# Kernel optimization log

Hardware: AMD Instinct MI355X
Metric: run time of the kernel (lower is better)

## Reference

```python
import jax, jax.numpy as jnp
import numpy as np

N, E, D, G = 50000, 600000, 128, 512  # nodes, edges, embed_dim, graphs-per-batch
LN_EPS = 1e-5


def setup_inputs() -> dict:
    key = jax.random.key(0)
    ks = jax.random.split(key, 8)
    node_hidden = jax.random.normal(ks[0], (N, D), dtype=jnp.float32)
    edge_hidden = jax.random.normal(ks[1], (E, D), dtype=jnp.float32)
    # GINEConv MLP params: Linear(D, 2D) -> ReLU -> Linear(2D, D)
    W1 = jax.random.normal(ks[2], (D, 2 * D), dtype=jnp.float32) * (1.0 / np.sqrt(D))
    b1 = jnp.zeros((2 * D,), dtype=jnp.float32)
    W2 = jax.random.normal(ks[3], (2 * D, D), dtype=jnp.float32) * (1.0 / np.sqrt(2 * D))
    b2 = jnp.zeros((D,), dtype=jnp.float32)
    ln_gamma = jnp.ones((D,), dtype=jnp.float32)
    ln_beta = jnp.zeros((D,), dtype=jnp.float32)
    edge_index = jax.random.randint(ks[4], (2, E), 0, N, dtype=jnp.int32)
    node_id = jnp.sort(jax.random.randint(ks[5], (N,), 0, G, dtype=jnp.int32))
    edge_id = jnp.sort(jax.random.randint(ks[6], (E,), 0, G, dtype=jnp.int32))
    return {
        "node_hidden": node_hidden, "edge_hidden": edge_hidden,
        "W1": W1, "b1": b1, "W2": W2, "b2": b2,
        "ln_gamma": ln_gamma, "ln_beta": ln_beta,
        "edge_index": edge_index, "node_id": node_id, "edge_id": edge_id,
    }


def reference(node_hidden, edge_hidden, W1, b1, W2, b2, ln_gamma, ln_beta,
              edge_index, node_id, edge_id):
    n = node_hidden.shape[0]
    src, dst = edge_index[0], edge_index[1]
    # --- GINEConv: msg = relu(x_src + e), scatter-add at dst, (1+eps)*x + agg, MLP ---
    msg = jax.nn.relu(node_hidden[src] + edge_hidden)          # [E, D]
    agg = jax.ops.segment_sum(msg, dst, num_segments=n)        # [N, D]
    h = node_hidden + agg                                      # eps = 0 (PyG default)
    h = jax.nn.relu(jnp.dot(h, W1) + b1)
    h = jnp.dot(h, W2) + b2                                    # [N, D]
    # --- LayerNorm over feature dim ---
    mu = jnp.mean(h, axis=-1, keepdims=True)
    var = jnp.mean(jnp.square(h - mu), axis=-1, keepdims=True)
    h = (h - mu) * jax.lax.rsqrt(var + LN_EPS) * ln_gamma + ln_beta
    # --- GraphNorm: divide each node's features by sqrt(#nodes in its graph) ---
    counts = jax.ops.segment_sum(jnp.ones((n,), dtype=h.dtype), node_id,
                                 num_segments=G)               # [G]
    scale = jax.lax.rsqrt(jnp.maximum(counts, 1.0))            # [G]
    h = h * scale[node_id][:, None]
    # --- last_act=True -> ReLU; dropout is identity in eval; residual add ---
    h = jax.nn.relu(h)
    return h + node_hidden
```

## Files before the change

kernel.cpp:

```cpp
#include <hip/hip_runtime.h>
#include <hip/hip_bf16.h>

#define N_NODES 50000
#define N_EDGES 600000
#define DIM     128
#define HID     256
#define NGRAPH  512
#define LN_EPS  1e-5f
#define CAP     48

typedef __attribute__((ext_vector_type(8))) short bf16x8;
typedef __attribute__((ext_vector_type(4))) float f32x4;

__device__ __forceinline__ unsigned short f2bf(float x) {
  unsigned int u = __builtin_bit_cast(unsigned int, x);
  unsigned int r = (u + 0x7FFFu + ((u >> 16) & 1u)) >> 16;
  return (unsigned short)r;
}

__global__ void k_init_prep(const float* __restrict__ W1, const float* __restrict__ W2,
                            unsigned char* __restrict__ blob,
                            int* __restrict__ deg, int* __restrict__ counts) {
  int id = blockIdx.x * 256 + threadIdx.x;
  if (id < N_NODES) deg[id] = 0;
  if (id < NGRAPH) counts[id] = 0;
  union { unsigned short s[8]; uint4 v; } u;
  if (id < 4096) {
    int c  = id >> 4;
    int k0 = (id & 15) * 8;
#pragma unroll
    for (int j = 0; j < 8; ++j) u.s[j] = f2bf(W1[(size_t)(k0 + j) * HID + c]);
    unsigned char* dst = blob + c * 256 + ((k0 * 2) ^ ((c & 7) << 4));
    *(uint4*)dst = u.v;
  } else if (id < 8192) {
    int id2 = id - 4096;
    int c  = id2 >> 5;
    int k0 = (id2 & 31) * 8;
#pragma unroll
    for (int j = 0; j < 8; ++j) u.s[j] = f2bf(W2[(size_t)(k0 + j) * DIM + c]);
    unsigned char* dst = blob + 65536 + c * 512 + ((k0 * 2) ^ ((c & 7) << 4));
    *(uint4*)dst = u.v;
  }
}

__global__ void k_scatter(const int* __restrict__ ei, const int* __restrict__ node_id,
                          int* __restrict__ deg, int2* __restrict__ slots2,
                          int* __restrict__ counts) {
  int t = blockIdx.x * 256 + threadIdx.x;
  if (t < N_NODES) atomicAdd(&counts[node_id[t]], 1);
  if (t < N_EDGES) {
    int src = ei[t];
    int dst = ei[N_EDGES + t];
    int pos = atomicAdd(&deg[dst], 1);
    if (pos < CAP) slots2[(size_t)dst * CAP + pos] = make_int2(t, src);
  }
}

__global__ __launch_bounds__(512) void k_gather(
    const f32x4* __restrict__ nh4, const f32x4* __restrict__ eh4,
    const int* __restrict__ deg, const int2* __restrict__ slots2,
    f32x4* __restrict__ out4) {
  const int lane = threadIdx.x & 63;
  const int wave = threadIdx.x >> 6;
  const int l31  = lane & 31;
  const int half = lane >> 5;
  const int nbase = (blockIdx.x * 8 + wave) * 4;

  int dcur = 0;
  int2 scur = make_int2(0, 0);
  if (nbase < N_NODES) {
    dcur = deg[nbase];
    if (lane < CAP) scur = slots2[(size_t)nbase * CAP + lane];
  }
#pragma unroll
  for (int p = 0; p < 4; ++p) {
    int node = nbase + p;
    if (node >= N_NODES) break;
    int d = min(dcur, CAP);
    int2 s = scur;
    if (p < 3) {
      int nn = nbase + p + 1;
      if (nn < N_NODES) {
        dcur = deg[nn];
        if (lane < CAP) scur = slots2[(size_t)nn * CAP + lane];
      } else {
        dcur = 0;
      }
    }
    f32x4 acc = (f32x4){0.f, 0.f, 0.f, 0.f};
    if (half == 0) acc = nh4[(size_t)node * 32 + l31];
    int nloop = (d + 1) >> 1;
#pragma unroll 4
    for (int i = 0; i < nloop; ++i) {
      int idx = 2 * i + half;
      int ee = __shfl(s.x, idx);
      int ss = __shfl(s.y, idx);
      if (idx < d) {
        f32x4 x = nh4[(size_t)ss * 32 + l31];
        f32x4 y = __builtin_nontemporal_load(&eh4[(size_t)ee * 32 + l31]);
        acc.x += fmaxf(x.x + y.x, 0.f);
        acc.y += fmaxf(x.y + y.y, 0.f);
        acc.z += fmaxf(x.z + y.z, 0.f);
        acc.w += fmaxf(x.w + y.w, 0.f);
      }
    }
    acc.x += __shfl_xor(acc.x, 32);
    acc.y += __shfl_xor(acc.y, 32);
    acc.z += __shfl_xor(acc.z, 32);
    acc.w += __shfl_xor(acc.w, 32);
    if (half == 0) out4[(size_t)node * 32 + l31] = acc;
  }
}

__global__ __launch_bounds__(512, 2) void k_mlp(
    const float* acc, const float* __restrict__ nh,
    const unsigned char* __restrict__ blob,
    const float* __restrict__ b1v, const float* __restrict__ b2v,
    const float* __restrict__ gam, const float* __restrict__ bet,
    const int* __restrict__ node_id, const int* __restrict__ counts,
    float* outp) {
  __shared__ unsigned char lds[131072];
  const int tid  = threadIdx.x;
  const int lane = tid & 63;
  const int wave = tid >> 6;
  const int l15  = lane & 15;
  const int lhi  = lane >> 4;
  const int swz  = (lane & 7) << 4;

  {
    const uint4* s = (const uint4*)blob;
    uint4* d = (uint4*)lds;
#pragma unroll
    for (int i = 0; i < 16; ++i) d[tid + i * 512] = s[tid + i * 512];
  }
  __syncthreads();

  const int row0 = blockIdx.x * 128 + wave * 16;
  const int arow = row0 + l15;
  const bool aok = arow < N_NODES;
  const float* ap = acc + (size_t)arow * DIM + lhi * 8;

  f32x4 c1[16];
#pragma unroll
  for (int i = 0; i < 16; ++i) c1[i] = (f32x4){0.f, 0.f, 0.f, 0.f};

#pragma unroll
  for (int ks = 0; ks < 4; ++ks) {
    bf16x8 af;
    if (aok) {
      float4 x0 = *(const float4*)(ap + ks * 32);
      float4 x1 = *(const float4*)(ap + ks * 32 + 4);
      af[0] = (short)f2bf(x0.x);
      af[1] = (short)f2bf(x0.y);
      af[2] = (short)f2bf(x0.z);
      af[3] = (short)f2bf(x0.w);
      af[4] = (short)f2bf(x1.x);
      af[5] = (short)f2bf(x1.y);
      af[6] = (short)f2bf(x1.z);
      af[7] = (short)f2bf(x1.w);
    } else {
#pragma unroll
      for (int j = 0; j < 8; ++j) af[j] = 0;
    }
#pragma unroll
    for (int ct = 0; ct < 16; ++ct) {
      int c = ct * 16 + l15;
      const bf16x8* bp = (const bf16x8*)(lds + c * 256 + ((ks * 64 + lhi * 16) ^ swz));
      c1[ct] = __builtin_amdgcn_mfma_f32_16x16x32_bf16(af, *bp, c1[ct], 0, 0, 0);
    }
  }
  __syncthreads();

  unsigned char* hb = lds + wave * 8192;
#pragma unroll
  for (int ct = 0; ct < 16; ++ct) {
    int c = ct * 16 + l15;
    float bb = b1v[c];
#pragma unroll
    for (int i = 0; i < 4; ++i) {
      int r = lhi * 4 + i;
      float v = fmaxf(c1[ct][i] + bb, 0.f);
      *(unsigned short*)(hb + r * 512 + ((2 * c) ^ ((r & 7) << 4))) = f2bf(v);
    }
  }
  __syncthreads();

  f32x4 c2[8];
#pragma unroll
  for (int i = 0; i < 8; ++i) c2[i] = (f32x4){0.f, 0.f, 0.f, 0.f};

#pragma unroll
  for (int ks = 0; ks < 8; ++ks) {
    bf16x8 af = *(const bf16x8*)(hb + l15 * 512 + ((ks * 64 + lhi * 16) ^ swz));
#pragma unroll
    for (int ct = 0; ct < 8; ++ct) {
      int c = ct * 16 + l15;
      const bf16x8* bp = (const bf16x8*)(lds + 65536 + c * 512 + ((ks * 64 + lhi * 16) ^ swz));
      c2[ct] = __builtin_amdgcn_mfma_f32_16x16x32_bf16(af, *bp, c2[ct], 0, 0, 0);
    }
  }

  float vbuf[8][4];
  float s[4] = {0.f, 0.f, 0.f, 0.f}, sq[4] = {0.f, 0.f, 0.f, 0.f};
#pragma unroll
  for (int ct = 0; ct < 8; ++ct) {
    float bb = b2v[ct * 16 + l15];
#pragma unroll
    for (int i = 0; i < 4; ++i) {
      float x = c2[ct][i] + bb;
      vbuf[ct][i] = x;
      s[i] += x;
      sq[i] += x * x;
    }
  }
#pragma unroll
  for (int m = 1; m <= 8; m <<= 1) {
#pragma unroll
    for (int i = 0; i < 4; ++i) {
      s[i] += __shfl_xor(s[i], m, 64);
      sq[i] += __shfl_xor(sq[i], m, 64);
    }
  }
  float mu[4], rstd[4], gs[4];
  int rr[4];
  bool rok[4];
#pragma unroll
  for (int i = 0; i < 4; ++i) {
    mu[i] = s[i] * (1.f / 128.f);
    float var = sq[i] * (1.f / 128.f) - mu[i] * mu[i];
    rstd[i] = rsqrtf(var + LN_EPS);
    rr[i] = row0 + lhi * 4 + i;
    rok[i] = rr[i] < N_NODES;
    int g = rok[i] ? node_id[rr[i]] : 0;
    gs[i] = rsqrtf(fmaxf((float)counts[g], 1.f));
  }
#pragma unroll
  for (int ct = 0; ct < 8; ++ct) {
    int c = ct * 16 + l15;
    float gg = gam[c], be = bet[c];
#pragma unroll
    for (int i = 0; i < 4; ++i) {
      if (rok[i]) {
        float y = (vbuf[ct][i] - mu[i]) * rstd[i] * gg + be;
        y *= gs[i];
        y = fmaxf(y, 0.f);
        y += nh[(size_t)rr[i] * DIM + c];
        outp[(size_t)rr[i] * DIM + c] = y;
      }
    }
  }
}

extern "C" void kernel_launch(void* const* d_in, const int* in_sizes, int n_in,
                              void* d_out, int out_size, void* d_ws, size_t ws_size,
                              hipStream_t stream) {
  const float* node_hidden = (const float*)d_in[0];
  const float* edge_hidden = (const float*)d_in[1];
  const float* W1  = (const float*)d_in[2];
  const float* b1  = (const float*)d_in[3];
  const float* W2  = (const float*)d_in[4];
  const float* b2  = (const float*)d_in[5];
  const float* lng = (const float*)d_in[6];
  const float* lnb = (const float*)d_in[7];
  const int* edge_index = (const int*)d_in[8];
  const int* node_id    = (const int*)d_in[9];
  float* out = (float*)d_out;

  unsigned char* ws = (unsigned char*)d_ws;
  unsigned char* blob = ws;
  int* counts   = (int*)(ws + 131072);
  int* deg      = (int*)(ws + 163840);
  int2* slots2  = (int2*)(ws + 393216);

  k_init_prep<<<196, 256, 0, stream>>>(W1, W2, blob, deg, counts);
  k_scatter<<<2344, 256, 0, stream>>>(edge_index, node_id, deg, slots2, counts);
  k_gather<<<1563, 512, 0, stream>>>((const f32x4*)node_hidden,
                                     (const f32x4*)edge_hidden,
                                     deg, slots2, (f32x4*)out);
  k_mlp<<<391, 512, 0, stream>>>(out, node_hidden, blob, b1, b2, lng, lnb,
                                 node_id, counts, out);
}
```

Measured before the change: 208.8 us.

## Gather node features in bf16 and hand bf16 aggregate to MLP

Adds a prep pass that converts node_hidden to bf16. The gather kernel then reads bf16 source-node rows instead of fp32, which halves that part of its random-gather traffic. The gather writes the aggregate as bf16 into a workspace buffer, so the MLP loads MFMA A-fragments directly without converting. This costs an extra full pass over node_hidden, and bf16 rounding of x_src before the relu and sum adds some error on top of the bf16 already used for the matmul input.

```diff
diff --git a/kernel.cpp b/kernel.cpp
--- a/kernel.cpp
+++ b/kernel.cpp
@@ -18,28 +18,42 @@
   return (unsigned short)r;
 }
 
-__global__ void k_init_prep(const float* __restrict__ W1, const float* __restrict__ W2,
-                            unsigned char* __restrict__ blob,
-                            int* __restrict__ deg, int* __restrict__ counts) {
+__device__ __forceinline__ float bf2f(unsigned int u) {
+  return __builtin_bit_cast(float, u << 16);
+}
+
+__global__ void k_prep(const float* __restrict__ W1, const float* __restrict__ W2,
+                       const float* __restrict__ nh,
+                       unsigned char* __restrict__ blob,
+                       unsigned short* __restrict__ nhb,
+                       int* __restrict__ deg, int* __restrict__ counts) {
   int id = blockIdx.x * 256 + threadIdx.x;
   if (id < N_NODES) deg[id] = 0;
   if (id < NGRAPH) counts[id] = 0;
-  union { unsigned short s[8]; uint4 v; } u;
+  if (id < (N_NODES * DIM) / 8) {
+    const float4* s = (const float4*)nh + (size_t)id * 2;
+    float4 a = s[0], b = s[1];
+    union { unsigned short s8[8]; uint4 v; } u;
+    u.s8[0] = f2bf(a.x); u.s8[1] = f2bf(a.y); u.s8[2] = f2bf(a.z); u.s8[3] = f2bf(a.w);
+    u.s8[4] = f2bf(b.x); u.s8[5] = f2bf(b.y); u.s8[6] = f2bf(b.z); u.s8[7] = f2bf(b.w);
+    *((uint4*)nhb + id) = u.v;
+  }
+  union { unsigned short s8[8]; uint4 v; } w;
   if (id < 4096) {
     int c  = id >> 4;
     int k0 = (id & 15) * 8;
 #pragma unroll
-    for (int j = 0; j < 8; ++j) u.s[j] = f2bf(W1[(size_t)(k0 + j) * HID + c]);
+    for (int j = 0; j < 8; ++j) w.s8[j] = f2bf(W1[(size_t)(k0 + j) * HID + c]);
     unsigned char* dst = blob + c * 256 + ((k0 * 2) ^ ((c & 7) << 4));
-    *(uint4*)dst = u.v;
+    *(uint4*)dst = w.v;
   } else if (id < 8192) {
     int id2 = id - 4096;
     int c  = id2 >> 5;
     int k0 = (id2 & 31) * 8;
 #pragma unroll
-    for (int j = 0; j < 8; ++j) u.s[j] = f2bf(W2[(size_t)(k0 + j) * DIM + c]);
+    for (int j = 0; j < 8; ++j) w.s8[j] = f2bf(W2[(size_t)(k0 + j) * DIM + c]);
     unsigned char* dst = blob + 65536 + c * 512 + ((k0 * 2) ^ ((c & 7) << 4));
-    *(uint4*)dst = u.v;
+    *(uint4*)dst = w.v;
   }
 }
 
@@ -58,13 +72,13 @@
 
 __global__ __launch_bounds__(512) void k_gather(
     const f32x4* __restrict__ nh4, const f32x4* __restrict__ eh4,
+    const uint2* __restrict__ nhb2,
     const int* __restrict__ deg, const int2* __restrict__ slots2,
-    f32x4* __restrict__ out4) {
+    uint2* __restrict__ hB2) {
   const int lane = threadIdx.x & 63;
-  const int wave = threadIdx.x >> 6;
   const int l31  = lane & 31;
   const int half = lane >> 5;
-  const int nbase = (blockIdx.x * 8 + wave) * 4;
+  const int nbase = (blockIdx.x * 8 + (threadIdx.x >> 6)) * 4;
 
   int dcur = 0;
   int2 scur = make_int2(0, 0);
@@ -96,29 +110,34 @@
       int ee = __shfl(s.x, idx);
       int ss = __shfl(s.y, idx);
       if (idx < d) {
-        f32x4 x = nh4[(size_t)ss * 32 + l31];
+        uint2 xb = nhb2[(size_t)ss * 32 + l31];
         f32x4 y = __builtin_nontemporal_load(&eh4[(size_t)ee * 32 + l31]);
-        acc.x += fmaxf(x.x + y.x, 0.f);
-        acc.y += fmaxf(x.y + y.y, 0.f);
-        acc.z += fmaxf(x.z + y.z, 0.f);
-        acc.w += fmaxf(x.w + y.w, 0.f);
+        acc.x += fmaxf(bf2f(xb.x & 0xffffu) + y.x, 0.f);
+        acc.y += fmaxf(bf2f(xb.x >> 16)     + y.y, 0.f);
+        acc.z += fmaxf(bf2f(xb.y & 0xffffu) + y.z, 0.f);
+        acc.w += fmaxf(bf2f(xb.y >> 16)     + y.w, 0.f);
       }
     }
     acc.x += __shfl_xor(acc.x, 32);
     acc.y += __shfl_xor(acc.y, 32);
     acc.z += __shfl_xor(acc.z, 32);
     acc.w += __shfl_xor(acc.w, 32);
-    if (half == 0) out4[(size_t)node * 32 + l31] = acc;
+    if (half == 0) {
+      uint2 o;
+      o.x = (unsigned)f2bf(acc.x) | ((unsigned)f2bf(acc.y) << 16);
+      o.y = (unsigned)f2bf(acc.z) | ((unsigned)f2bf(acc.w) << 16);
+      hB2[(size_t)node * 32 + l31] = o;
+    }
   }
 }
 
 __global__ __launch_bounds__(512, 2) void k_mlp(
-    const float* acc, const float* __restrict__ nh,
+    const unsigned char* __restrict__ hB, const float* __restrict__ nh,
     const unsigned char* __restrict__ blob,
     const float* __restrict__ b1v, const float* __restrict__ b2v,
     const float* __restrict__ gam, const float* __restrict__ bet,
     const int* __restrict__ node_id, const int* __restrict__ counts,
-    float* outp) {
+    float* __restrict__ outp) {
   __shared__ unsigned char lds[131072];
   const int tid  = threadIdx.x;
   const int lane = tid & 63;
@@ -138,7 +157,6 @@
   const int row0 = blockIdx.x * 128 + wave * 16;
   const int arow = row0 + l15;
   const bool aok = arow < N_NODES;
-  const float* ap = acc + (size_t)arow * DIM + lhi * 8;
 
   f32x4 c1[16];
 #pragma unroll
@@ -146,22 +164,8 @@
 
 #pragma unroll
   for (int ks = 0; ks < 4; ++ks) {
-    bf16x8 af;
-    if (aok) {
-      float4 x0 = *(const float4*)(ap + ks * 32);
-      float4 x1 = *(const float4*)(ap + ks * 32 + 4);
-      af[0] = (short)f2bf(x0.x);
-      af[1] = (short)f2bf(x0.y);
-      af[2] = (short)f2bf(x0.z);
-      af[3] = (short)f2bf(x0.w);
-      af[4] = (short)f2bf(x1.x);
-      af[5] = (short)f2bf(x1.y);
-      af[6] = (short)f2bf(x1.z);
-      af[7] = (short)f2bf(x1.w);
-    } else {
-#pragma unroll
-      for (int j = 0; j < 8; ++j) af[j] = 0;
-    }
+    bf16x8 af = (bf16x8){0, 0, 0, 0, 0, 0, 0, 0};
+    if (aok) af = *(const bf16x8*)(hB + (size_t)arow * 256 + ks * 64 + lhi * 16);
 #pragma unroll
     for (int ct = 0; ct < 16; ++ct) {
       int c = ct * 16 + l15;
@@ -271,12 +275,15 @@
   int* counts   = (int*)(ws + 131072);
   int* deg      = (int*)(ws + 163840);
   int2* slots2  = (int2*)(ws + 393216);
-
-  k_init_prep<<<196, 256, 0, stream>>>(W1, W2, blob, deg, counts);
+  unsigned short* nhb = (unsigned short*)(ws + 33554432);
+  unsigned char*  hB  = ws + 50331648;
+
+  k_prep<<<3126, 256, 0, stream>>>(W1, W2, node_hidden, blob, nhb, deg, counts);
   k_scatter<<<2344, 256, 0, stream>>>(edge_index, node_id, deg, slots2, counts);
   k_gather<<<1563, 512, 0, stream>>>((const f32x4*)node_hidden,
                                      (const f32x4*)edge_hidden,
-                                     deg, slots2, (f32x4*)out);
-  k_mlp<<<391, 512, 0, stream>>>(out, node_hidden, blob, b1, b2, lng, lnb,
+                                     (const uint2*)nhb,
+                                     deg, slots2, (uint2*)hB);
+  k_mlp<<<391, 512, 0, stream>>>(hB, node_hidden, blob, b1, b2, lng, lnb,
                                  node_id, counts, out);
 }
```

Result: faster. 190.0 us (-9.0%).
